# Performance work log

Hardware: AMD Instinct MI355X
Metric: run time of the kernel (lower is better)

Reference implementation:

```python
import jax, jax.numpy as jnp
import numpy as np

B, T, S, H, D = 2, 2048, 2048, 16, 64
E = H * D  # embed_dim = 1024


def setup_inputs() -> dict:
    key = jax.random.key(0)
    k1, k2, k3, k4 = jax.random.split(key, 4)
    q = jax.random.normal(k1, (B, T, H, D), jnp.float32)
    kv = jax.random.normal(k2, (B, S, 2, H, D), jnp.float32)
    # nn.MultiheadAttention packed in-projection (xavier-ish scale) and out-projection
    in_proj_w = jax.random.normal(k3, (3 * E, E), jnp.float32) * (1.0 / np.sqrt(E)).astype(np.float32)
    in_proj_b = jnp.zeros((3 * E,), jnp.float32)
    out_proj_w = jax.random.normal(k4, (E, E), jnp.float32) * (1.0 / np.sqrt(E)).astype(np.float32)
    out_proj_b = jnp.zeros((E,), jnp.float32)
    return {"q": q, "kv": kv, "in_proj_w": in_proj_w, "in_proj_b": in_proj_b,
            "out_proj_w": out_proj_w, "out_proj_b": out_proj_b}


def reference(q, kv, in_proj_w, in_proj_b, out_proj_w, out_proj_b):
    Bq, Tq, Hh, Dd = q.shape
    Ss = kv.shape[1]
    Ee = Hh * Dd
    # flatten heads: q -> (B,T,E); kv unbinds k (two=0) and v (two=1)
    qf = q.reshape(Bq, Tq, Ee)
    kf = kv[:, :, 0].reshape(Bq, Ss, Ee)
    vf = kv[:, :, 1].reshape(Bq, Ss, Ee)
    wq, wk, wv = jnp.split(in_proj_w, 3, axis=0)
    bq, bk, bv = jnp.split(in_proj_b, 3)
    qp = (qf @ wq.T + bq).reshape(Bq, Tq, Hh, Dd).transpose(0, 2, 1, 3)  # bhtd
    kp = (kf @ wk.T + bk).reshape(Bq, Ss, Hh, Dd).transpose(0, 2, 1, 3)  # bhsd
    vp = (vf @ wv.T + bv).reshape(Bq, Ss, Hh, Dd).transpose(0, 2, 1, 3)  # bhsd
    scale = 1.0 / jnp.sqrt(jnp.asarray(Dd, qp.dtype))
    scores = jnp.einsum('bhtd,bhsd->bhts', qp, kp) * scale
    attn = jax.nn.softmax(scores, axis=-1)  # full SxS materialization, as in non-fused MHA
    ctx = jnp.einsum('bhts,bhsd->bhtd', attn, vp)
    ctx = ctx.transpose(0, 2, 1, 3).reshape(Bq, Tq, Ee)
    out = (ctx @ out_proj_w.T + out_proj_b).reshape(Bq, Tq, Hh, Dd)
    # need_weights=True default: weights averaged over heads -> (B,T,S)
    attn_weights = attn.mean(axis=1)
    return out, attn_weights
```

## Files before the change

### kernel.cpp

```cpp
#include <hip/hip_runtime.h>
#include <math.h>

#define Bb 2
#define Tt 2048
#define Ssz 2048
#define Hh 16
#define Dd 64
#define Ee 1024

#define NQ  (Bb*Tt*Ee)
#define NKV (Bb*Ssz*Ee)
#define NW  (3*Ee*Ee)
#define NWO (Ee*Ee)

#define LOG2E 1.44269504088896f

typedef __bf16 bf16x8 __attribute__((ext_vector_type(8)));
typedef float  floatx4 __attribute__((ext_vector_type(4)));
typedef short  short4_ __attribute__((ext_vector_type(4)));
typedef unsigned short u16;
typedef unsigned int   u32;

__device__ __forceinline__ u16 f2bf(float f) {
    __bf16 h = (__bf16)f;
    union { __bf16 h; u16 u; } v; v.h = h; return v.u;
}
__device__ __forceinline__ float bf2f(u16 b) {
    union { u32 u; float f; } v; v.u = ((u32)b) << 16; return v.f;
}
__device__ __forceinline__ float load_f(const void* p, int i, bool isbf) {
    if (isbf) return bf2f(((const u16*)p)[i]);
    return ((const float*)p)[i];
}
__device__ __forceinline__ u32 load2(const void* p, int i, bool isbf) {
    if (isbf) return ((const u32*)p)[i >> 1];
    float2 f = ((const float2*)p)[i >> 1];
    return (u32)f2bf(f.x) | ((u32)f2bf(f.y) << 16);
}

typedef __attribute__((address_space(1))) const unsigned int gas_u32;
typedef __attribute__((address_space(3))) unsigned int las_u32;
__device__ __forceinline__ void gl_lds16(const u16* g, u16* l) {
    __builtin_amdgcn_global_load_lds((gas_u32*)g, (las_u32*)l, 16, 0, 0);
}

__device__ __forceinline__ int swz(int k, int row) {
    return (k & ~63) | ((((k >> 3) ^ row) & 7) << 3) | (k & 7);
}

__global__ void k_detect(const u32* __restrict__ qw, int* __restrict__ flag) {
    __shared__ int cnt;
    if (threadIdx.x == 0) cnt = 0;
    __syncthreads();
    int h = 0;
    for (int i = threadIdx.x; i < 4096; i += 256) {
        u32 w = qw[i];
        u32 b = (w >> 8) & 0x7Fu;
        if ((b & 0x7Cu) == 0x3Cu) h++;
    }
    atomicAdd(&cnt, h);
    __syncthreads();
    if (threadIdx.x == 0) flag[0] = (cnt > 2048) ? 1 : 0;
}

__global__ void k_pack(const void* __restrict__ q, const void* __restrict__ kv,
                       const void* __restrict__ w_in, const void* __restrict__ b_in,
                       const void* __restrict__ w_out, const void* __restrict__ b_out,
                       const int* __restrict__ flag,
                       u32* __restrict__ qb, u32* __restrict__ kb, u32* __restrict__ vb,
                       u32* __restrict__ wb, u32* __restrict__ wob, float* __restrict__ biases) {
    bool isbf = flag[0] != 0;
    int i = (blockIdx.x * 256 + threadIdx.x) * 2;
    if (i < NQ) { int row = i >> 10, k = i & 1023;
        qb[(((size_t)row << 10) | (u32)swz(k, row)) >> 1] = load2(q, i, isbf); return; }
    i -= NQ;
    if (i < NKV) { int row = i >> 10, e = i & 1023;
        kb[(((size_t)row << 10) | (u32)swz(e, row)) >> 1] = load2(kv, row*2048 + e, isbf); return; }
    i -= NKV;
    if (i < NKV) { int row = i >> 10, e = i & 1023;
        vb[(((size_t)row << 10) | (u32)swz(e, row)) >> 1] = load2(kv, row*2048 + 1024 + e, isbf); return; }
    i -= NKV;
    if (i < NW) { int row = i >> 10, k = i & 1023;
        wb[(((size_t)row << 10) | (u32)swz(k, row)) >> 1] = load2(w_in, i, isbf); return; }
    i -= NW;
    if (i < NWO) { int row = i >> 10, k = i & 1023;
        wob[(((size_t)row << 10) | (u32)swz(k, row)) >> 1] = load2(w_out, i, isbf); return; }
    i -= NWO;
    if (i < 3072) { biases[i] = load_f(b_in, i, isbf); biases[i+1] = load_f(b_in, i+1, isbf); return; }
    i -= 3072;
    if (i < 1024) { biases[3072+i] = load_f(b_out, i, isbf); biases[3072+i+1] = load_f(b_out, i+1, isbf); }
}

__device__ __forceinline__ void gemm128(const u16* __restrict__ Ab, const u16* __restrict__ Wb,
                                        u16* As, u16* Ws, floatx4 (&acc)[4][4], int tid) {
    int lane = tid & 63, w = tid >> 6, q = lane >> 4, ml = lane & 15;
    int mh = (w >> 1) * 64, nh = (w & 1) * 64;
    int rs = tid >> 3, cs = (tid & 7) * 8;
#pragma unroll
    for (int j = 0; j < 4; ++j) {
        gl_lds16(Ab + (size_t)(j*32 + rs) * 1024 + cs, &As[(j*32 + rs)*64 + cs]);
        gl_lds16(Wb + (size_t)(j*32 + rs) * 1024 + cs, &Ws[(j*32 + rs)*64 + cs]);
    }
    __syncthreads();
    int cur = 0;
    for (int k0 = 0; k0 < 1024; k0 += 64) {
        if (k0 + 64 < 1024) {
            int nb = (cur ^ 1) * 8192;
#pragma unroll
            for (int j = 0; j < 4; ++j) {
                gl_lds16(Ab + (size_t)(j*32 + rs) * 1024 + k0 + 64 + cs, &As[nb + (j*32 + rs)*64 + cs]);
                gl_lds16(Wb + (size_t)(j*32 + rs) * 1024 + k0 + 64 + cs, &Ws[nb + (j*32 + rs)*64 + cs]);
            }
        }
        const u16* Asc = As + cur * 8192;
        const u16* Wsc = Ws + cur * 8192;
#pragma unroll
        for (int kk = 0; kk < 2; ++kk) {
            int gs = (((kk*4 + q) ^ ml) & 7) * 8;
            bf16x8 af[4], bfv[4];
#pragma unroll
            for (int mt = 0; mt < 4; ++mt) af[mt]  = *(const bf16x8*)&Asc[(mh + mt*16 + ml)*64 + gs];
#pragma unroll
            for (int nt = 0; nt < 4; ++nt) bfv[nt] = *(const bf16x8*)&Wsc[(nh + nt*16 + ml)*64 + gs];
#pragma unroll
            for (int mt = 0; mt < 4; ++mt)
#pragma unroll
                for (int nt = 0; nt < 4; ++nt)
                    acc[mt][nt] = __builtin_amdgcn_mfma_f32_16x16x32_bf16(af[mt], bfv[nt], acc[mt][nt], 0, 0, 0);
        }
        __syncthreads();
        cur ^= 1;
    }
}

__global__ __launch_bounds__(256) void k_gemm_qkv(const u16* __restrict__ qb, const u16* __restrict__ kb,
                                                  const u16* __restrict__ vb, const u16* __restrict__ wb,
                                                  const float* __restrict__ biases,
                                                  u16* __restrict__ Qp, u16* __restrict__ Kp,
                                                  u16* __restrict__ Vt) {
    __shared__ u16 As[2 * 128 * 64];
    __shared__ u16 Ws[2 * 128 * 64];
    int flat = blockIdx.x + 8 * (blockIdx.y + 32 * blockIdx.z);
    int wg = (flat & 7) * 96 + (flat >> 3);
    int mode = wg >> 8;
    int rem = wg & 255;
    int m0 = (rem >> 3) * 128;
    int n0 = (rem & 7) * 128;
    const u16* A = (mode == 0) ? qb : (mode == 1) ? kb : vb;
    const u16* W = wb + (size_t)mode * Ee * Ee;
    const float* bias = biases + mode * 1024;
    int tid = threadIdx.x, lane = tid & 63;
    int w = tid >> 6, q = lane >> 4, ml = lane & 15;
    int mh = (w >> 1) * 64, nh = (w & 1) * 64;

    floatx4 acc[4][4];
#pragma unroll
    for (int a = 0; a < 4; ++a)
#pragma unroll
        for (int b2 = 0; b2 < 4; ++b2) acc[a][b2] = (floatx4){0.f, 0.f, 0.f, 0.f};

    gemm128(A + (size_t)m0 * 1024, W + (size_t)n0 * 1024, As, Ws, acc, tid);

#pragma unroll
    for (int mt = 0; mt < 4; ++mt) {
#pragma unroll
        for (int nt = 0; nt < 4; ++nt) {
#pragma unroll
            for (int rg = 0; rg < 4; ++rg) {
                int m = m0 + mh + mt*16 + q*4 + rg;
                int n = n0 + nh + nt*16 + ml;
                float val = acc[mt][nt][rg] + bias[n];
                int b = m >> 11, t = m & 2047, hh = n >> 6, d = n & 63;
                if (mode == 0) {
                    int dsw = ((((d >> 3) ^ t) & 7) << 3) | (d & 7);
                    Qp[((size_t)(b*16 + hh) * 2048 + t) * 64 + dsw] = f2bf(val * (0.125f * LOG2E));
                } else if (mode == 1) {
                    int dsw = ((((d >> 3) ^ t) & 7) << 3) | (d & 7);
                    Kp[((size_t)(b*16 + hh) * 2048 + t) * 64 + dsw] = f2bf(val);
                } else {
                    int tsw = (t & ~63) | ((((t >> 3) ^ d) & 7) << 3) | (t & 7);
                    Vt[((size_t)(b*16 + hh) * 64 + d) * 2048 + tsw] = f2bf(val);
                }
            }
        }
    }
}

__global__ __launch_bounds__(256) void k_gemm_out(const u16* __restrict__ A, const u16* __restrict__ W,
                                                  const float* __restrict__ bias, void* __restrict__ Cout,
                                                  const int* __restrict__ flag) {
    __shared__ u16 As[2 * 128 * 64];
    __shared__ u16 Ws[2 * 128 * 64];
    int flat = blockIdx.x + 8 * blockIdx.y;
    int wg = (flat & 7) * 32 + (flat >> 3);
    int m0 = (wg >> 3) * 128;
    int n0 = (wg & 7) * 128;
    int tid = threadIdx.x, lane = tid & 63;
    int w = tid >> 6, q = lane >> 4, ml = lane & 15;
    int mh = (w >> 1) * 64, nh = (w & 1) * 64;

    floatx4 acc[4][4];
#pragma unroll
    for (int a = 0; a < 4; ++a)
#pragma unroll
        for (int b2 = 0; b2 < 4; ++b2) acc[a][b2] = (floatx4){0.f, 0.f, 0.f, 0.f};

    gemm128(A + (size_t)m0 * 1024, W + (size_t)n0 * 1024, As, Ws, acc, tid);

    bool outbf = flag[0] != 0;
#pragma unroll
    for (int mt = 0; mt < 4; ++mt) {
#pragma unroll
        for (int nt = 0; nt < 4; ++nt) {
#pragma unroll
            for (int rg = 0; rg < 4; ++rg) {
                int m = m0 + mh + mt*16 + q*4 + rg;
                int n = n0 + nh + nt*16 + ml;
                float val = acc[mt][nt][rg] + bias[n];
                if (outbf) ((u16*)Cout)[(size_t)m * 1024 + n] = f2bf(val);
                else       ((float*)Cout)[(size_t)m * 1024 + n] = val;
            }
        }
    }
}

__global__ __launch_bounds__(512) void k_flash(const u16* __restrict__ Qp, const u16* __restrict__ Kp,
                                               const u16* __restrict__ Vt, u16* __restrict__ ctx,
                                               float* __restrict__ lbuf) {
    __shared__ u16 smem[3 * 64 * 128];
    u16* Qs = smem;
    u16* KsB = smem + 8192;
    u16* VsB = smem + 16384;
    int t0 = blockIdx.x * 128;
    int h  = blockIdx.y;
    int b  = blockIdx.z;
    const u16* Qh = Qp + (size_t)(b*16 + h) * 2048 * 64;
    const u16* Kh = Kp + (size_t)(b*16 + h) * 2048 * 64;
    const u16* Vh = Vt + (size_t)(b*16 + h) * 64 * 2048;
    int tid = threadIdx.x, lane = tid & 63;
    int wv = tid >> 6, r = wv & 3, e = wv >> 2;
    int q = lane >> 4, ml = lane & 15;
    int rsw = tid >> 3, cs = (tid & 7) * 8;

#pragma unroll
    for (int j = 0; j < 2; ++j)
        gl_lds16(Qh + (size_t)(t0 + j*64 + rsw) * 64 + cs, &Qs[(j*64 + rsw)*64 + cs]);
    gl_lds16(Kh + (size_t)rsw * 64 + cs, &KsB[rsw*64 + cs]);
    gl_lds16(Vh + (size_t)rsw * 2048 + cs, &VsB[rsw*64 + cs]);
    __syncthreads();

    bf16x8 qf[2][2];
#pragma unroll
    for (int mt = 0; mt < 2; ++mt)
#pragma unroll
        for (int kk = 0; kk < 2; ++kk)
            qf[mt][kk] = *(const bf16x8*)&Qs[(r*32 + mt*16 + ml)*64 + (((kk*4 + q) ^ ml) & 7)*8];

    float lp[2] = {0.f, 0.f};
    floatx4 ct[2][4];
#pragma unroll
    for (int mt = 0; mt < 2; ++mt)
#pragma unroll
        for (int i = 0; i < 4; ++i) ct[mt][i] = (floatx4){0.f, 0.f, 0.f, 0.f};

    int cur = 0;
    for (int s0 = 0; s0 < 2048; s0 += 64) {
        if (s0 + 64 < 2048) {
            gl_lds16(Kh + (size_t)(s0 + 64 + rsw) * 64 + cs, &KsB[(cur ^ 1)*4096 + rsw*64 + cs]);
            gl_lds16(Vh + (size_t)rsw * 2048 + (s0 + 64) + cs, &VsB[(cur ^ 1)*4096 + rsw*64 + cs]);
        }
        const u16* Ksc = KsB + cur*4096;
        const u16* Vsc = VsB + cur*4096;

        floatx4 sc[2][2];
#pragma unroll
        for (int mt = 0; mt < 2; ++mt)
#pragma unroll
            for (int i = 0; i < 2; ++i) sc[mt][i] = (floatx4){0.f, 0.f, 0.f, 0.f};
#pragma unroll
        for (int kk = 0; kk < 2; ++kk) {
            int gs = (((kk*4 + q) ^ ml) & 7) * 8;
#pragma unroll
            for (int ntl = 0; ntl < 2; ++ntl) {
                bf16x8 kf = *(const bf16x8*)&Ksc[(e*32 + ntl*16 + ml)*64 + gs];
#pragma unroll
                for (int mt = 0; mt < 2; ++mt)
                    sc[mt][ntl] = __builtin_amdgcn_mfma_f32_16x16x32_bf16(kf, qf[mt][kk], sc[mt][ntl], 0, 0, 0);
            }
        }

        short4_ pa[2][2];
#pragma unroll
        for (int mt = 0; mt < 2; ++mt) {
#pragma unroll
            for (int ntl = 0; ntl < 2; ++ntl) {
#pragma unroll
                for (int rg = 0; rg < 4; ++rg) {
                    float p = __builtin_amdgcn_exp2f(sc[mt][ntl][rg]);
                    lp[mt] += p;
                    pa[mt][ntl][rg] = (short)f2bf(p);
                }
            }
        }

#pragma unroll
        for (int ksl = 0; ksl < 2; ++ksl) {
#pragma unroll
            for (int nt = 0; nt < 4; ++nt) {
                const u16* vp = &Vsc[(nt*16 + ml)*64
                                     + (((((e*2 + ksl)*2 + (q >> 1)) ^ ml) & 7) << 3) + (q & 1)*4];
                short4_ vf = *(const short4_*)vp;
#pragma unroll
                for (int mt = 0; mt < 2; ++mt)
                    ct[mt][nt] = __builtin_amdgcn_mfma_f32_16x16x16bf16_1k(pa[mt][ksl], vf, ct[mt][nt], 0, 0, 0);
            }
        }

        __syncthreads();
        cur ^= 1;
    }

#pragma unroll
    for (int mt = 0; mt < 2; ++mt) {
        lp[mt] += __shfl_xor(lp[mt], 16);
        lp[mt] += __shfl_xor(lp[mt], 32);
    }

    float* redc = (float*)(smem + 8192);
    float* redl = (float*)smem;
    int basec = r*2048 + lane*32;
    if (e == 1) {
#pragma unroll
        for (int mt = 0; mt < 2; ++mt)
#pragma unroll
            for (int nt = 0; nt < 4; ++nt) {
                int g = mt*4 + nt;
                *(floatx4*)&redc[basec + ((g ^ (lane & 7)) << 2)] = ct[mt][nt];
            }
        redl[(r*64 + lane)*2]     = lp[0];
        redl[(r*64 + lane)*2 + 1] = lp[1];
    }
    __syncthreads();
    if (e == 0) {
#pragma unroll
        for (int mt = 0; mt < 2; ++mt)
#pragma unroll
            for (int nt = 0; nt < 4; ++nt) {
                int g = mt*4 + nt;
                ct[mt][nt] += *(const floatx4*)&redc[basec + ((g ^ (lane & 7)) << 2)];
            }
        lp[0] += redl[(r*64 + lane)*2];
        lp[1] += redl[(r*64 + lane)*2 + 1];

        if (lane < 16) {
            size_t base = (size_t)(b*16 + h) * 2048 + t0 + r*32;
#pragma unroll
            for (int mt = 0; mt < 2; ++mt) lbuf[base + mt*16 + lane] = lp[mt];
        }

#pragma unroll
        for (int mt = 0; mt < 2; ++mt) {
            float il[4];
#pragma unroll
            for (int rg = 0; rg < 4; ++rg) il[rg] = 1.f / __shfl(lp[mt], q*4 + rg);
#pragma unroll
            for (int nt = 0; nt < 4; ++nt) {
#pragma unroll
                for (int rg = 0; rg < 4; ++rg) {
                    int t = t0 + r*32 + mt*16 + q*4 + rg;
                    int c64 = nt*16 + ml;
                    int col = h*64 + (((((c64 >> 3) ^ t) & 7)) << 3) + (c64 & 7);
                    ctx[(size_t)(b*2048 + t) * 1024 + col] = f2bf(ct[mt][nt][rg] * il[rg]);
                }
            }
        }
    }
}

__global__ __launch_bounds__(256) void k_attnw(const u16* __restrict__ Qp, const u16* __restrict__ Kp,
                                               const float* __restrict__ lbuf,
                                               void* __restrict__ dout, const int* __restrict__ flag) {
    __shared__ u16 Qs[64 * 64];
    __shared__ u16 Ks[128 * 64];
    int s0 = blockIdx.x * 128;
    int t0 = blockIdx.y * 64;
    int b  = blockIdx.z;
    int tid = threadIdx.x, lane = tid & 63;
    int w = tid >> 6, q = lane >> 4, ml = lane & 15;
    int rsw = tid >> 3, cs = (tid & 7) * 8;

    floatx4 aw[8];
#pragma unroll
    for (int i = 0; i < 8; ++i) aw[i] = (floatx4){0.f, 0.f, 0.f, 0.f};

    for (int h = 0; h < 16; ++h) {
        const u16* Qh = Qp + (size_t)(b*16 + h) * 2048 * 64;
        const u16* Kh = Kp + (size_t)(b*16 + h) * 2048 * 64;
        __syncthreads();
#pragma unroll
        for (int j = 0; j < 2; ++j)
            gl_lds16(Qh + (size_t)(t0 + j*32 + rsw) * 64 + cs, &Qs[(j*32 + rsw)*64 + cs]);
#pragma unroll
        for (int j = 0; j < 4; ++j)
            gl_lds16(Kh + (size_t)(s0 + j*32 + rsw) * 64 + cs, &Ks[(j*32 + rsw)*64 + cs]);
        __syncthreads();

        float il[4];
        size_t sb = (size_t)(b*16 + h) * 2048 + t0 + w*16 + q*4;
#pragma unroll
        for (int rg = 0; rg < 4; ++rg) il[rg] = 1.f / lbuf[sb + rg];

        floatx4 sc[8];
#pragma unroll
        for (int i = 0; i < 8; ++i) sc[i] = (floatx4){0.f, 0.f, 0.f, 0.f};
#pragma unroll
        for (int kk = 0; kk < 2; ++kk) {
            int gs = (((kk*4 + q) ^ ml) & 7) * 8;
            bf16x8 qfr = *(const bf16x8*)&Qs[(w*16 + ml)*64 + gs];
#pragma unroll
            for (int nt = 0; nt < 8; ++nt) {
                bf16x8 kfr = *(const bf16x8*)&Ks[(nt*16 + ml)*64 + gs];
                sc[nt] = __builtin_amdgcn_mfma_f32_16x16x32_bf16(qfr, kfr, sc[nt], 0, 0, 0);
            }
        }
#pragma unroll
        for (int nt = 0; nt < 8; ++nt)
#pragma unroll
            for (int rg = 0; rg < 4; ++rg)
                aw[nt][rg] += __builtin_amdgcn_exp2f(sc[nt][rg]) * il[rg];
    }

    bool outbf = flag[0] != 0;
    const size_t attn_base = (size_t)Bb * Tt * Ee;
#pragma unroll
    for (int nt = 0; nt < 8; ++nt) {
#pragma unroll
        for (int rg = 0; rg < 4; ++rg) {
            int t = t0 + w*16 + q*4 + rg;
            int s = s0 + nt*16 + ml;
            float val = aw[nt][rg] * 0.0625f;
            size_t idx = attn_base + (size_t)(b*2048 + t) * 2048 + s;
            if (outbf) ((u16*)dout)[idx] = f2bf(val);
            else       ((float*)dout)[idx] = val;
        }
    }
}

extern "C" void kernel_launch(void* const* d_in, const int* in_sizes, int n_in,
                              void* d_out, int out_size, void* d_ws, size_t ws_size,
                              hipStream_t stream) {
    const void* q     = d_in[0];
    const void* kv    = d_in[1];
    const void* w_in  = d_in[2];
    const void* b_in  = d_in[3];
    const void* w_out = d_in[4];
    const void* b_out = d_in[5];

    char* ws = (char*)d_ws;
    size_t off = 0;
    auto alloc = [&](size_t bytes) -> void* {
        void* p = ws + off;
        off += (bytes + 255) & ~(size_t)255;
        return p;
    };
    int*   flag   = (int*)alloc(256);
    u16*   qb     = (u16*)alloc((size_t)NQ * 2);
    u16*   kb     = (u16*)alloc((size_t)NKV * 2);
    u16*   vb     = (u16*)alloc((size_t)NKV * 2);
    u16*   wb     = (u16*)alloc((size_t)NW * 2);
    u16*   wob    = (u16*)alloc((size_t)NWO * 2);
    float* biases = (float*)alloc(4096 * 4);
    u16*   Qp     = (u16*)alloc((size_t)NQ * 2);
    u16*   Kp     = (u16*)alloc((size_t)NKV * 2);
    u16*   Vt     = (u16*)alloc((size_t)NKV * 2);
    u16*   ctx    = (u16*)alloc((size_t)NQ * 2);
    float* lbuf   = (float*)alloc((size_t)Bb * Hh * Tt * 4);

    k_detect<<<1, 256, 0, stream>>>((const u32*)q, flag);

    int totalPairs = (NQ + NKV + NKV + NW + NWO + 4096) / 2;
    k_pack<<<(totalPairs + 255) / 256, 256, 0, stream>>>(q, kv, w_in, b_in, w_out, b_out, flag,
                                                         (u32*)qb, (u32*)kb, (u32*)vb,
                                                         (u32*)wb, (u32*)wob, biases);

    k_gemm_qkv<<<dim3(8, 32, 3), 256, 0, stream>>>(qb, kb, vb, wb, biases, Qp, Kp, Vt);

    k_flash<<<dim3(Tt / 128, Hh, Bb), 512, 0, stream>>>(Qp, Kp, Vt, ctx, lbuf);
    k_attnw<<<dim3(Ssz / 128, Tt / 64, Bb), 256, 0, stream>>>(Qp, Kp, lbuf, d_out, flag);

    k_gemm_out<<<dim3(8, 32), 256, 0, stream>>>(ctx, wob, biases + 3072, d_out, flag);
}
```

Measured before the change: 281.9 us.

## Split QKV GEMM K-dimension across two wave groups with LDS reduction

The QKV projection kernel now launches 512 threads per block. Each half of the block computes a 128x128 tile over half of the K=1024 reduction, single-buffered with syncs around each load. The two partial accumulators are then summed through LDS before the epilogue. The aim is more waves per CU and more memory parallelism for a grid of only 768 blocks. The cost is dropping the double-buffer prefetch, adding extra barriers and a reduction pass, and leaving half the threads idle in the epilogue.

Result: slower. 290.8 us (+3.2%).

```diff
diff --git a/kernel.cpp b/kernel.cpp
--- a/kernel.cpp
+++ b/kernel.cpp
@@ -91,8 +91,8 @@
     if (i < 1024) { biases[3072+i] = load_f(b_out, i, isbf); biases[3072+i+1] = load_f(b_out, i+1, isbf); }
 }
 
-__device__ __forceinline__ void gemm128(const u16* __restrict__ Ab, const u16* __restrict__ Wb,
-                                        u16* As, u16* Ws, floatx4 (&acc)[4][4], int tid) {
+__device__ __forceinline__ void gemm128_dbuf(const u16* __restrict__ Ab, const u16* __restrict__ Wb,
+                                             u16* As, u16* Ws, floatx4 (&acc)[4][4], int tid) {
     int lane = tid & 63, w = tid >> 6, q = lane >> 4, ml = lane & 15;
     int mh = (w >> 1) * 64, nh = (w & 1) * 64;
     int rs = tid >> 3, cs = (tid & 7) * 8;
@@ -133,25 +133,33 @@
     }
 }
 
-__global__ __launch_bounds__(256) void k_gemm_qkv(const u16* __restrict__ qb, const u16* __restrict__ kb,
-                                                  const u16* __restrict__ vb, const u16* __restrict__ wb,
-                                                  const float* __restrict__ biases,
-                                                  u16* __restrict__ Qp, u16* __restrict__ Kp,
-                                                  u16* __restrict__ Vt) {
-    __shared__ u16 As[2 * 128 * 64];
-    __shared__ u16 Ws[2 * 128 * 64];
+__global__ __launch_bounds__(512, 4) void k_gemm_qkv(const u16* __restrict__ qb, const u16* __restrict__ kb,
+                                                     const u16* __restrict__ vb, const u16* __restrict__ wb,
+                                                     const float* __restrict__ biases,
+                                                     u16* __restrict__ Qp, u16* __restrict__ Kp,
+                                                     u16* __restrict__ Vt) {
+    __shared__ u16 smem[4 * 8192];
     int flat = blockIdx.x + 8 * (blockIdx.y + 32 * blockIdx.z);
     int wg = (flat & 7) * 96 + (flat >> 3);
     int mode = wg >> 8;
     int rem = wg & 255;
     int m0 = (rem >> 3) * 128;
     int n0 = (rem & 7) * 128;
-    const u16* A = (mode == 0) ? qb : (mode == 1) ? kb : vb;
-    const u16* W = wb + (size_t)mode * Ee * Ee;
+    const u16* A = ((mode == 0) ? qb : (mode == 1) ? kb : vb) + (size_t)m0 * 1024;
+    const u16* W = wb + (size_t)mode * Ee * Ee + (size_t)n0 * 1024;
     const float* bias = biases + mode * 1024;
-    int tid = threadIdx.x, lane = tid & 63;
-    int w = tid >> 6, q = lane >> 4, ml = lane & 15;
-    int mh = (w >> 1) * 64, nh = (w & 1) * 64;
+    int tid = threadIdx.x;
+    int half = tid >> 8;
+    int t256 = tid & 255;
+    int lane = tid & 63;
+    int w4 = (tid >> 6) & 3;
+    int q = lane >> 4, ml = lane & 15;
+    int mh = (w4 >> 1) * 64, nh = (w4 & 1) * 64;
+    int rs = t256 >> 3, cs = (t256 & 7) * 8;
+    u16* AsH = smem + half * 8192;
+    u16* WsH = smem + 16384 + half * 8192;
+    const u16* Ah = A + half * 512;
+    const u16* Wh = W + half * 512;
 
     floatx4 acc[4][4];
 #pragma unroll
@@ -159,27 +167,68 @@
 #pragma unroll
         for (int b2 = 0; b2 < 4; ++b2) acc[a][b2] = (floatx4){0.f, 0.f, 0.f, 0.f};
 
-    gemm128(A + (size_t)m0 * 1024, W + (size_t)n0 * 1024, As, Ws, acc, tid);
-
-#pragma unroll
-    for (int mt = 0; mt < 4; ++mt) {
-#pragma unroll
-        for (int nt = 0; nt < 4; ++nt) {
-#pragma unroll
-            for (int rg = 0; rg < 4; ++rg) {
-                int m = m0 + mh + mt*16 + q*4 + rg;
-                int n = n0 + nh + nt*16 + ml;
-                float val = acc[mt][nt][rg] + bias[n];
-                int b = m >> 11, t = m & 2047, hh = n >> 6, d = n & 63;
-                if (mode == 0) {
-                    int dsw = ((((d >> 3) ^ t) & 7) << 3) | (d & 7);
-                    Qp[((size_t)(b*16 + hh) * 2048 + t) * 64 + dsw] = f2bf(val * (0.125f * LOG2E));
-                } else if (mode == 1) {
-                    int dsw = ((((d >> 3) ^ t) & 7) << 3) | (d & 7);
-                    Kp[((size_t)(b*16 + hh) * 2048 + t) * 64 + dsw] = f2bf(val);
-                } else {
-                    int tsw = (t & ~63) | ((((t >> 3) ^ d) & 7) << 3) | (t & 7);
-                    Vt[((size_t)(b*16 + hh) * 64 + d) * 2048 + tsw] = f2bf(val);
+    for (int k0 = 0; k0 < 512; k0 += 64) {
+        __syncthreads();
+#pragma unroll
+        for (int j = 0; j < 4; ++j) {
+            gl_lds16(Ah + (size_t)(j*32 + rs) * 1024 + k0 + cs, &AsH[(j*32 + rs)*64 + cs]);
+            gl_lds16(Wh + (size_t)(j*32 + rs) * 1024 + k0 + cs, &WsH[(j*32 + rs)*64 + cs]);
+        }
+        __syncthreads();
+#pragma unroll
+        for (int kk = 0; kk < 2; ++kk) {
+            int gs = (((kk*4 + q) ^ ml) & 7) * 8;
+            bf16x8 af[4], bfv[4];
+#pragma unroll
+            for (int mt = 0; mt < 4; ++mt) af[mt]  = *(const bf16x8*)&AsH[(mh + mt*16 + ml)*64 + gs];
+#pragma unroll
+            for (int nt = 0; nt < 4; ++nt) bfv[nt] = *(const bf16x8*)&WsH[(nh + nt*16 + ml)*64 + gs];
+#pragma unroll
+            for (int mt = 0; mt < 4; ++mt)
+#pragma unroll
+                for (int nt = 0; nt < 4; ++nt)
+                    acc[mt][nt] = __builtin_amdgcn_mfma_f32_16x16x32_bf16(af[mt], bfv[nt], acc[mt][nt], 0, 0, 0);
+        }
+    }
+    __syncthreads();
+
+    float* redf = (float*)smem;
+    int rbase = t256 * 64;
+    if (half == 1) {
+#pragma unroll
+        for (int mt = 0; mt < 4; ++mt)
+#pragma unroll
+            for (int nt = 0; nt < 4; ++nt)
+                *(floatx4*)&redf[rbase + (((mt*4 + nt) ^ (t256 & 15)) << 2)] = acc[mt][nt];
+    }
+    __syncthreads();
+    if (half == 0) {
+#pragma unroll
+        for (int mt = 0; mt < 4; ++mt)
+#pragma unroll
+            for (int nt = 0; nt < 4; ++nt)
+                acc[mt][nt] += *(const floatx4*)&redf[rbase + (((mt*4 + nt) ^ (t256 & 15)) << 2)];
+
+#pragma unroll
+        for (int mt = 0; mt < 4; ++mt) {
+#pragma unroll
+            for (int nt = 0; nt < 4; ++nt) {
+#pragma unroll
+                for (int rg = 0; rg < 4; ++rg) {
+                    int m = m0 + mh + mt*16 + q*4 + rg;
+                    int n = n0 + nh + nt*16 + ml;
+                    float val = acc[mt][nt][rg] + bias[n];
+                    int b = m >> 11, t = m & 2047, hh = n >> 6, d = n & 63;
+                    if (mode == 0) {
+                        int dsw = ((((d >> 3) ^ t) & 7) << 3) | (d & 7);
+                        Qp[((size_t)(b*16 + hh) * 2048 + t) * 64 + dsw] = f2bf(val * (0.125f * LOG2E));
+                    } else if (mode == 1) {
+                        int dsw = ((((d >> 3) ^ t) & 7) << 3) | (d & 7);
+                        Kp[((size_t)(b*16 + hh) * 2048 + t) * 64 + dsw] = f2bf(val);
+                    } else {
+                        int tsw = (t & ~63) | ((((t >> 3) ^ d) & 7) << 3) | (t & 7);
+                        Vt[((size_t)(b*16 + hh) * 64 + d) * 2048 + tsw] = f2bf(val);
+                    }
                 }
             }
         }
@@ -205,7 +254,7 @@
 #pragma unroll
         for (int b2 = 0; b2 < 4; ++b2) acc[a][b2] = (floatx4){0.f, 0.f, 0.f, 0.f};
 
-    gemm128(A + (size_t)m0 * 1024, W + (size_t)n0 * 1024, As, Ws, acc, tid);
+    gemm128_dbuf(A + (size_t)m0 * 1024, W + (size_t)n0 * 1024, As, Ws, acc, tid);
 
     bool outbf = flag[0] != 0;
 #pragma unroll
@@ -483,7 +532,7 @@
                                                          (u32*)qb, (u32*)kb, (u32*)vb,
                                                          (u32*)wb, (u32*)wob, biases);
 
-    k_gemm_qkv<<<dim3(8, 32, 3), 256, 0, stream>>>(qb, kb, vb, wb, biases, Qp, Kp, Vt);
+    k_gemm_qkv<<<dim3(8, 32, 3), 512, 0, stream>>>(qb, kb, vb, wb, biases, Qp, Kp, Vt);
 
     k_flash<<<dim3(Tt / 128, Hh, Bb), 512, 0, stream>>>(Qp, Kp, Vt, ctx, lbuf);
     k_attnw<<<dim3(Ssz / 128, Tt / 64, Bb), 256, 0, stream>>>(Qp, Kp, lbuf, d_out, flag);
```

## Enlarge QKV GEMM and attention-weights tiles to 512-thread blocks

Applied to the files above, without the earlier changes.

The QKV projection now uses 256x128 tiles with 8 waves per block and a single-buffered K loop, in place of the double-buffered 128x128 tile with 4 waves. The head-averaged attention-weights kernel now covers 128 query rows per block with 8 waves, so each K tile is loaded once for twice as many rows. Both changes aim to cut global/LDS reloads and launch a smaller grid. In exchange the QKV GEMM loses its load/compute overlap and the grid has fewer blocks per CU.

After: 277.3 us. No clear change (-1.6%).

```diff
diff --git a/kernel.cpp b/kernel.cpp
--- a/kernel.cpp
+++ b/kernel.cpp
@@ -91,8 +91,8 @@
     if (i < 1024) { biases[3072+i] = load_f(b_out, i, isbf); biases[3072+i+1] = load_f(b_out, i+1, isbf); }
 }
 
-__device__ __forceinline__ void gemm128(const u16* __restrict__ Ab, const u16* __restrict__ Wb,
-                                        u16* As, u16* Ws, floatx4 (&acc)[4][4], int tid) {
+__device__ __forceinline__ void gemm128_dbuf(const u16* __restrict__ Ab, const u16* __restrict__ Wb,
+                                             u16* As, u16* Ws, floatx4 (&acc)[4][4], int tid) {
     int lane = tid & 63, w = tid >> 6, q = lane >> 4, ml = lane & 15;
     int mh = (w >> 1) * 64, nh = (w & 1) * 64;
     int rs = tid >> 3, cs = (tid & 7) * 8;
@@ -133,25 +133,27 @@
     }
 }
 
-__global__ __launch_bounds__(256) void k_gemm_qkv(const u16* __restrict__ qb, const u16* __restrict__ kb,
+__global__ __launch_bounds__(512) void k_gemm_qkv(const u16* __restrict__ qb, const u16* __restrict__ kb,
                                                   const u16* __restrict__ vb, const u16* __restrict__ wb,
                                                   const float* __restrict__ biases,
                                                   u16* __restrict__ Qp, u16* __restrict__ Kp,
                                                   u16* __restrict__ Vt) {
-    __shared__ u16 As[2 * 128 * 64];
-    __shared__ u16 Ws[2 * 128 * 64];
-    int flat = blockIdx.x + 8 * (blockIdx.y + 32 * blockIdx.z);
-    int wg = (flat & 7) * 96 + (flat >> 3);
-    int mode = wg >> 8;
-    int rem = wg & 255;
-    int m0 = (rem >> 3) * 128;
+    __shared__ u16 As[256 * 64];
+    __shared__ u16 Ws[128 * 64];
+    int flat = blockIdx.x + 8 * (blockIdx.y + 16 * blockIdx.z);
+    int wg = (flat & 7) * 48 + (flat >> 3);
+    int mode = wg >> 7;
+    int rem = wg & 127;
+    int m0 = (rem >> 3) * 256;
     int n0 = (rem & 7) * 128;
-    const u16* A = (mode == 0) ? qb : (mode == 1) ? kb : vb;
-    const u16* W = wb + (size_t)mode * Ee * Ee;
+    const u16* A = ((mode == 0) ? qb : (mode == 1) ? kb : vb) + (size_t)m0 * 1024;
+    const u16* W = wb + (size_t)mode * Ee * Ee + (size_t)n0 * 1024;
     const float* bias = biases + mode * 1024;
     int tid = threadIdx.x, lane = tid & 63;
-    int w = tid >> 6, q = lane >> 4, ml = lane & 15;
+    int w = tid >> 6;
+    int q = lane >> 4, ml = lane & 15;
     int mh = (w >> 1) * 64, nh = (w & 1) * 64;
+    int rs = tid >> 3, cs = (tid & 7) * 8;
 
     floatx4 acc[4][4];
 #pragma unroll
@@ -159,7 +161,30 @@
 #pragma unroll
         for (int b2 = 0; b2 < 4; ++b2) acc[a][b2] = (floatx4){0.f, 0.f, 0.f, 0.f};
 
-    gemm128(A + (size_t)m0 * 1024, W + (size_t)n0 * 1024, As, Ws, acc, tid);
+    for (int k0 = 0; k0 < 1024; k0 += 64) {
+        __syncthreads();
+#pragma unroll
+        for (int j = 0; j < 4; ++j)
+            gl_lds16(A + (size_t)(j*64 + rs) * 1024 + k0 + cs, &As[(j*64 + rs)*64 + cs]);
+#pragma unroll
+        for (int j = 0; j < 2; ++j)
+            gl_lds16(W + (size_t)(j*64 + rs) * 1024 + k0 + cs, &Ws[(j*64 + rs)*64 + cs]);
+        __syncthreads();
+#pragma unroll
+        for (int kk = 0; kk < 2; ++kk) {
+            int gs = (((kk*4 + q) ^ ml) & 7) * 8;
+            bf16x8 af[4], bfv[4];
+#pragma unroll
+            for (int mt = 0; mt < 4; ++mt) af[mt]  = *(const bf16x8*)&As[(mh + mt*16 + ml)*64 + gs];
+#pragma unroll
+            for (int nt = 0; nt < 4; ++nt) bfv[nt] = *(const bf16x8*)&Ws[(nh + nt*16 + ml)*64 + gs];
+#pragma unroll
+            for (int mt = 0; mt < 4; ++mt)
+#pragma unroll
+                for (int nt = 0; nt < 4; ++nt)
+                    acc[mt][nt] = __builtin_amdgcn_mfma_f32_16x16x32_bf16(af[mt], bfv[nt], acc[mt][nt], 0, 0, 0);
+        }
+    }
 
 #pragma unroll
     for (int mt = 0; mt < 4; ++mt) {
@@ -205,7 +230,7 @@
 #pragma unroll
         for (int b2 = 0; b2 < 4; ++b2) acc[a][b2] = (floatx4){0.f, 0.f, 0.f, 0.f};
 
-    gemm128(A + (size_t)m0 * 1024, W + (size_t)n0 * 1024, As, Ws, acc, tid);
+    gemm128_dbuf(A + (size_t)m0 * 1024, W + (size_t)n0 * 1024, As, Ws, acc, tid);
 
     bool outbf = flag[0] != 0;
 #pragma unroll
@@ -377,13 +402,13 @@
     }
 }
 
-__global__ __launch_bounds__(256) void k_attnw(const u16* __restrict__ Qp, const u16* __restrict__ Kp,
+__global__ __launch_bounds__(512) void k_attnw(const u16* __restrict__ Qp, const u16* __restrict__ Kp,
                                                const float* __restrict__ lbuf,
                                                void* __restrict__ dout, const int* __restrict__ flag) {
-    __shared__ u16 Qs[64 * 64];
+    __shared__ u16 Qs[128 * 64];
     __shared__ u16 Ks[128 * 64];
     int s0 = blockIdx.x * 128;
-    int t0 = blockIdx.y * 64;
+    int t0 = blockIdx.y * 128;
     int b  = blockIdx.z;
     int tid = threadIdx.x, lane = tid & 63;
     int w = tid >> 6, q = lane >> 4, ml = lane & 15;
@@ -398,11 +423,10 @@
         const u16* Kh = Kp + (size_t)(b*16 + h) * 2048 * 64;
         __syncthreads();
 #pragma unroll
-        for (int j = 0; j < 2; ++j)
-            gl_lds16(Qh + (size_t)(t0 + j*32 + rsw) * 64 + cs, &Qs[(j*32 + rsw)*64 + cs]);
-#pragma unroll
-        for (int j = 0; j < 4; ++j)
-            gl_lds16(Kh + (size_t)(s0 + j*32 + rsw) * 64 + cs, &Ks[(j*32 + rsw)*64 + cs]);
+        for (int j = 0; j < 2; ++j) {
+            gl_lds16(Qh + (size_t)(t0 + j*64 + rsw) * 64 + cs, &Qs[(j*64 + rsw)*64 + cs]);
+            gl_lds16(Kh + (size_t)(s0 + j*64 + rsw) * 64 + cs, &Ks[(j*64 + rsw)*64 + cs]);
+        }
         __syncthreads();
 
         float il[4];
@@ -483,10 +507,10 @@
                                                          (u32*)qb, (u32*)kb, (u32*)vb,
                                                          (u32*)wb, (u32*)wob, biases);
 
-    k_gemm_qkv<<<dim3(8, 32, 3), 256, 0, stream>>>(qb, kb, vb, wb, biases, Qp, Kp, Vt);
+    k_gemm_qkv<<<dim3(8, 16, 3), 512, 0, stream>>>(qb, kb, vb, wb, biases, Qp, Kp, Vt);
 
     k_flash<<<dim3(Tt / 128, Hh, Bb), 512, 0, stream>>>(Qp, Kp, Vt, ctx, lbuf);
-    k_attnw<<<dim3(Ssz / 128, Tt / 64, Bb), 256, 0, stream>>>(Qp, Kp, lbuf, d_out, flag);
+    k_attnw<<<dim3(Ssz / 128, Tt / 128, Bb), 512, 0, stream>>>(Qp, Kp, lbuf, d_out, flag);
 
     k_gemm_out<<<dim3(8, 32), 256, 0, stream>>>(ctx, wob, biases + 3072, d_out, flag);
 }
```
